# Optimization experiments

Measured on AMD Instinct MI355X. Metric: run time of the kernel, lower is better.

The kernel has to match this reference:

```python
import jax, jax.numpy as jnp
import numpy as np

N = 50000      # nodes
E = 500000     # edges
IN_FEAT = 128
OUT_FEAT = 128
R = 200        # num_relations
NB = 16        # num_bases -> 8x8 blocks
SI = IN_FEAT // NB   # submat_in = 8
SO = OUT_FEAT // NB  # submat_out = 8


def setup_inputs() -> dict:
    key = jax.random.key(0)
    k1, k2, k3, k4, k5, k6, k7 = jax.random.split(key, 7)
    h = jax.random.normal(k1, (N, IN_FEAT), dtype=jnp.float32)
    norm = jax.random.uniform(k2, (N, 1), dtype=jnp.float32)
    weight = jax.random.normal(k3, (R, NB * SI * SO), dtype=jnp.float32) * 0.1
    loop_weight = jax.random.normal(k4, (IN_FEAT, OUT_FEAT), dtype=jnp.float32) * 0.1
    src = jax.random.randint(k5, (E,), 0, N, dtype=jnp.int32)
    dst = jax.random.randint(k6, (E,), 0, N, dtype=jnp.int32)
    etype = jax.random.randint(k7, (E,), 0, R, dtype=jnp.int32)
    return {"h": h, "norm": norm, "weight": weight, "loop_weight": loop_weight,
            "src": src, "dst": dst, "etype": etype}


def reference(h, norm, weight, loop_weight, src, dst, etype):
    # self-loop message: [N, out_feat]
    loop_message = h @ loop_weight
    # per-edge relation-weight gather: [E, NB, SI, SO]
    w_e = weight[etype].reshape(-1, NB, SI, SO)
    # src features as per-basis blocks: [E, NB, SI]
    x_e = h[src].reshape(-1, NB, SI)
    # block-diagonal bmm -> messages [E, out_feat]
    msg = jnp.einsum('ebi,ebio->ebo', x_e, w_e).reshape(-1, OUT_FEAT)
    # scatter-sum to destination nodes (fn.sum(msg -> h))
    agg = jax.ops.segment_sum(msg, dst, num_segments=N)
    # apply_func: multiply by per-node norm, then add self-loop and activation
    nodes = agg * norm
    nodes = nodes + loop_message
    return jax.nn.relu(nodes)
```

## Files before the change

kernel.cpp:

```cpp
#include <hip/hip_runtime.h>
#include <hip/hip_bf16.h>


#define IN_FEAT 128
#define OUT_FEAT 128
#define SCAN_CHUNK 512

using short8  = __attribute__((ext_vector_type(8))) short;
using float4v = __attribute__((ext_vector_type(4))) float;

__device__ inline float blo(unsigned u) { return __uint_as_float(u << 16); }
__device__ inline float bhi(unsigned u) { return __uint_as_float(u & 0xffff0000u); }
__device__ inline unsigned short f2bf(float f) {
  __hip_bfloat16 b = __float2bfloat16(f);
  return *reinterpret_cast<unsigned short*>(&b);
}

__device__ inline float dot2bf(unsigned x, unsigned w, float c) {
#if __has_builtin(__builtin_amdgcn_fdot2_f32_bf16)
  typedef __bf16 bf16x2 __attribute__((ext_vector_type(2)));
  return __builtin_amdgcn_fdot2_f32_bf16(__builtin_bit_cast(bf16x2, x),
                                         __builtin_bit_cast(bf16x2, w), c, false);
#else
  return c + blo(x) * blo(w) + bhi(x) * bhi(w);
#endif
}

__global__ __launch_bounds__(256) void k_prep(
    const float* __restrict__ w, unsigned short* __restrict__ w16, int wtotal,
    const float* __restrict__ h, uint4* __restrict__ h16p, int htotal8,
    const float* __restrict__ lw, unsigned short* __restrict__ lwT,
    const int* __restrict__ dst, int* __restrict__ cnt, int E,
    int bw, int bh, int blw) {
  const int bid = blockIdx.x;
  if (bid < bw) {
    const int idx = bid * 256 + threadIdx.x;
    if (idx < wtotal) {
      const int r = idx >> 10;
      const int rem = idx & 1023;
      const int b = rem >> 6;
      const int q = rem & 63;
      const int opp = q >> 4;
      const int t = q & 15;
      const int j = t >> 3;
      const int i = t & 7;
      w16[idx] = f2bf(w[((size_t)r << 10) + b * 64 + i * 8 + opp * 2 + j]);
    }
  } else if (bid < bw + bh) {
    const int t = (bid - bw) * 256 + threadIdx.x;
    if (t < htotal8) {
      const float4 a = ((const float4*)h)[2 * t];
      const float4 b = ((const float4*)h)[2 * t + 1];
      uint4 o;
      o.x = (unsigned)f2bf(a.x) | ((unsigned)f2bf(a.y) << 16);
      o.y = (unsigned)f2bf(a.z) | ((unsigned)f2bf(a.w) << 16);
      o.z = (unsigned)f2bf(b.x) | ((unsigned)f2bf(b.y) << 16);
      o.w = (unsigned)f2bf(b.z) | ((unsigned)f2bf(b.w) << 16);
      h16p[t] = o;
    }
  } else if (bid < bw + bh + blw) {
    const int idx = (bid - bw - bh) * 256 + threadIdx.x;
    if (idx < IN_FEAT * OUT_FEAT) {
      const int o = idx >> 7;
      const int k = idx & 127;
      lwT[idx] = f2bf(lw[k * 128 + o]);
    }
  } else {
    const int e = (bid - bw - bh - blw) * 256 + threadIdx.x;
    if (e < E) atomicAdd(&cnt[dst[e]], 1);
  }
}

__global__ __launch_bounds__(256) void gemm_mfma(
    const unsigned short* __restrict__ h16, const unsigned short* __restrict__ lwT,
    float* __restrict__ out, int N) {
  const int wid = threadIdx.x >> 6;
  const int lane = threadIdx.x & 63;
  const int row0 = blockIdx.x * 64 + wid * 16;
  if (row0 >= N) return;
  const int m = lane & 15;
  const int kg = (lane >> 4) * 8;
  const int arow = min(row0 + m, N - 1);

  float4v acc[8];
  #pragma unroll
  for (int nt = 0; nt < 8; ++nt) acc[nt] = (float4v){0.f, 0.f, 0.f, 0.f};

  const unsigned short* ap = h16 + (size_t)arow * 128 + kg;
  const unsigned short* bp = lwT + (size_t)m * 128 + kg;

  #pragma unroll
  for (int kc = 0; kc < 4; ++kc) {
    const short8 a = *(const short8*)(ap + kc * 32);
    #pragma unroll
    for (int nt = 0; nt < 8; ++nt) {
      const short8 b = *(const short8*)(bp + nt * 2048 + kc * 32);
      acc[nt] = __builtin_amdgcn_mfma_f32_16x16x32_bf16(a, b, acc[nt], 0, 0, 0);
    }
  }

  const int crow = row0 + (lane >> 4) * 4;
  #pragma unroll
  for (int nt = 0; nt < 8; ++nt) {
    #pragma unroll
    for (int r = 0; r < 4; ++r) {
      const int row = crow + r;
      if (row < N) out[(size_t)row * 128 + nt * 16 + m] = acc[nt][r];
    }
  }
}

__global__ __launch_bounds__(256) void k_hist(
    const int* __restrict__ dst, int* __restrict__ cnt, int E) {
  const int e = blockIdx.x * blockDim.x + threadIdx.x;
  if (e < E) atomicAdd(&cnt[dst[e]], 1);
}

__global__ __launch_bounds__(256) void k_chunksum(
    const int* __restrict__ cnt, int* __restrict__ bsum, int N) {
  __shared__ int s[256];
  const int t = threadIdx.x;
  const int base = blockIdx.x * SCAN_CHUNK;
  int v = 0;
  int i0 = base + t, i1 = base + 256 + t;
  if (i0 < N) v += cnt[i0];
  if (i1 < N) v += cnt[i1];
  s[t] = v;
  __syncthreads();
  for (int d = 128; d > 0; d >>= 1) {
    if (t < d) s[t] += s[t + d];
    __syncthreads();
  }
  if (t == 0) bsum[blockIdx.x] = s[0];
}

__global__ void k_scanb(int* __restrict__ bsum, int nblk) {
  const int lane = threadIdx.x;
  if (nblk <= 128) {
    int o0 = (lane < nblk) ? bsum[lane] : 0;
    int o1 = (64 + lane < nblk) ? bsum[64 + lane] : 0;
    int v0 = o0, v1 = o1;
    #pragma unroll
    for (int d = 1; d < 64; d <<= 1) {
      int t0 = __shfl_up(v0, d);
      int t1 = __shfl_up(v1, d);
      if (lane >= d) { v0 += t0; v1 += t1; }
    }
    const int total0 = __shfl(v0, 63);
    if (lane < nblk) bsum[lane] = v0 - o0;
    if (64 + lane < nblk) bsum[64 + lane] = total0 + v1 - o1;
  } else if (lane == 0) {
    int run = 0;
    for (int b = 0; b < nblk; ++b) { int v = bsum[b]; bsum[b] = run; run += v; }
  }
}

__global__ __launch_bounds__(256) void k_offsets(
    const int* __restrict__ cnt, const int* __restrict__ bsum,
    int* __restrict__ pos, int N) {
  __shared__ int s[256];
  const int t = threadIdx.x;
  const int base = blockIdx.x * SCAN_CHUNK;
  const int i0 = base + 2 * t;
  const int i1 = i0 + 1;
  const int c0 = (i0 < N) ? cnt[i0] : 0;
  const int c1 = (i1 < N) ? cnt[i1] : 0;
  const int pair = c0 + c1;
  s[t] = pair;
  __syncthreads();
  #pragma unroll
  for (int d = 1; d < 256; d <<= 1) {
    int v = (t >= d) ? s[t - d] : 0;
    __syncthreads();
    s[t] += v;
    __syncthreads();
  }
  const int ex = s[t] - pair + bsum[blockIdx.x];
  if (i0 < N) pos[i0] = ex;
  if (i1 < N) pos[i1] = ex + c0;
}

__global__ __launch_bounds__(256) void k_scatter(
    const int* __restrict__ src, const int* __restrict__ dst,
    const int* __restrict__ etype, int* __restrict__ pos,
    int2* __restrict__ srcet, int E) {
  const int e = blockIdx.x * blockDim.x + threadIdx.x;
  if (e < E) {
    const int p = atomicAdd(&pos[dst[e]], 1);
    srcet[p] = make_int2(src[e], etype[e]);
  }
}

__global__ __launch_bounds__(256) void agg_bf16(
    const unsigned short* __restrict__ h16, const float* __restrict__ norm,
    const unsigned short* __restrict__ w16, const int* __restrict__ pos,
    const int* __restrict__ cnt, const int2* __restrict__ srcet,
    float* __restrict__ out, int N) {
  const int node = (int)((blockIdx.x * blockDim.x + threadIdx.x) >> 6);
  const int lane = threadIdx.x & 63;
  if (node >= N) return;

  const int b = lane >> 2;
  const int opp = lane & 3;
  const int woff = b * 64 + opp * 16;
  const int hoff = b * 8;

  const int num = cnt[node];
  const int end = pos[node];
  const int begin = end - num;

  float a0 = 0.f, a1 = 0.f;

  for (int base = 0; base < num; base += 64) {
    const int cn = min(64, num - base);
    const int2 my = srcet[begin + base + min(lane, cn - 1)];
    #pragma unroll 4
    for (int i = 0; i < cn; ++i) {
      const int s = __shfl(my.x, i);
      const int r = __shfl(my.y, i);
      const unsigned short* wp = w16 + ((size_t)r << 10) + woff;
      const uint4 wa = *(const uint4*)(wp);
      const uint4 wb = *(const uint4*)(wp + 8);
      const uint4 xv = *(const uint4*)(h16 + ((size_t)s << 7) + hoff);

      a0 = dot2bf(xv.x, wa.x, a0);
      a0 = dot2bf(xv.y, wa.y, a0);
      a0 = dot2bf(xv.z, wa.z, a0);
      a0 = dot2bf(xv.w, wa.w, a0);
      a1 = dot2bf(xv.x, wb.x, a1);
      a1 = dot2bf(xv.y, wb.y, a1);
      a1 = dot2bf(xv.z, wb.z, a1);
      a1 = dot2bf(xv.w, wb.w, a1);
    }
  }

  const float nm = norm[node];
  const int o = b * 8 + opp * 2;
  float* outp = out + ((size_t)node << 7) + o;
  float2 prev = *(const float2*)outp;
  float2 res;
  res.x = fmaxf(prev.x + a0 * nm, 0.f);
  res.y = fmaxf(prev.y + a1 * nm, 0.f);
  *(float2*)outp = res;
}

__global__ __launch_bounds__(256) void selfloop_gemm(
    const float* __restrict__ h, const float* __restrict__ lw,
    float* __restrict__ out, int n) {
  __shared__ float slw[IN_FEAT * OUT_FEAT];
  __shared__ float sh[32 * IN_FEAT];

  {
    const float4* s4 = (const float4*)lw;
    float4* d4 = (float4*)slw;
    for (int i = threadIdx.x; i < IN_FEAT * OUT_FEAT / 4; i += 256) d4[i] = s4[i];
  }

  const int cg = threadIdx.x & 31;
  const int rg = threadIdx.x >> 5;

  for (int base = blockIdx.x * 32; base < n; base += gridDim.x * 32) {
    const int nrows = min(32, n - base);
    __syncthreads();
    {
      const float4* hs = (const float4*)(h + (size_t)base * IN_FEAT);
      float4* sd = (float4*)sh;
      const int cnt = nrows * (IN_FEAT / 4);
      for (int i = threadIdx.x; i < cnt; i += 256) sd[i] = hs[i];
    }
    __syncthreads();

    float4 acc[4];
    #pragma unroll
    for (int j = 0; j < 4; ++j) acc[j] = make_float4(0.f, 0.f, 0.f, 0.f);

    #pragma unroll 4
    for (int k = 0; k < IN_FEAT; ++k) {
      const float4 w = ((const float4*)slw)[k * 32 + cg];
      #pragma unroll
      for (int j = 0; j < 4; ++j) {
        const float hv = sh[(rg + 8 * j) * IN_FEAT + k];
        acc[j].x += hv * w.x;
        acc[j].y += hv * w.y;
        acc[j].z += hv * w.z;
        acc[j].w += hv * w.w;
      }
    }

    #pragma unroll
    for (int j = 0; j < 4; ++j) {
      const int r = rg + 8 * j;
      if (r < nrows) {
        ((float4*)(out + (size_t)(base + r) * OUT_FEAT))[cg] = acc[j];
      }
    }
  }
}

__global__ __launch_bounds__(256) void agg(
    const float* __restrict__ h, const float* __restrict__ norm,
    const float* __restrict__ weight, const int* __restrict__ pos,
    const int* __restrict__ cnt, const int2* __restrict__ srcet,
    float* __restrict__ out, int N) {
  const int node = (int)((blockIdx.x * blockDim.x + threadIdx.x) >> 6);
  const int lane = threadIdx.x & 63;
  if (node >= N) return;

  const int b = lane >> 2;
  const int op = (lane & 3) * 2;
  const int boff = b * 64 + op;

  const int num = cnt[node];
  const int end = pos[node];
  const int begin = end - num;

  float a0 = 0.f, a1 = 0.f;

  for (int base = 0; base < num; base += 64) {
    const int cn = min(64, num - base);
    const int2 my = srcet[begin + base + min(lane, cn - 1)];
    #pragma unroll 2
    for (int i = 0; i < cn; ++i) {
      const int s = __shfl(my.x, i);
      const int r = __shfl(my.y, i);
      const float* xp = h + ((size_t)s << 7) + b * 8;
      const float4 x0 = ((const float4*)xp)[0];
      const float4 x1 = ((const float4*)xp)[1];
      const float* wp = weight + ((size_t)r << 10) + boff;
      const float2 w0 = *(const float2*)(wp);
      const float2 w1 = *(const float2*)(wp + 8);
      const float2 w2 = *(const float2*)(wp + 16);
      const float2 w3 = *(const float2*)(wp + 24);
      const float2 w4 = *(const float2*)(wp + 32);
      const float2 w5 = *(const float2*)(wp + 40);
      const float2 w6 = *(const float2*)(wp + 48);
      const float2 w7 = *(const float2*)(wp + 56);
      a0 += x0.x * w0.x; a1 += x0.x * w0.y;
      a0 += x0.y * w1.x; a1 += x0.y * w1.y;
      a0 += x0.z * w2.x; a1 += x0.z * w2.y;
      a0 += x0.w * w3.x; a1 += x0.w * w3.y;
      a0 += x1.x * w4.x; a1 += x1.x * w4.y;
      a0 += x1.y * w5.x; a1 += x1.y * w5.y;
      a0 += x1.z * w6.x; a1 += x1.z * w6.y;
      a0 += x1.w * w7.x; a1 += x1.w * w7.y;
    }
  }

  const float nm = norm[node];
  const int o = b * 8 + op;
  float* outp = out + ((size_t)node << 7) + o;
  float2 prev = *(const float2*)outp;
  float2 res;
  res.x = fmaxf(prev.x + a0 * nm, 0.f);
  res.y = fmaxf(prev.y + a1 * nm, 0.f);
  *(float2*)outp = res;
}

__global__ __launch_bounds__(256) void edge_msg(
    const float* __restrict__ h, const float* __restrict__ norm,
    const float* __restrict__ weight, const int* __restrict__ src,
    const int* __restrict__ dst, const int* __restrict__ etype,
    float* out, int E) {
  const int wave = (int)((blockIdx.x * blockDim.x + threadIdx.x) >> 6);
  const int lane = threadIdx.x & 63;
  if (wave >= E) return;

  const int s = src[wave];
  const int d = dst[wave];
  const int r = etype[wave];
  const float nrm = norm[d];

  const int b = lane >> 2;
  const int op = (lane & 3) * 2;

  const float* xp = h + (size_t)s * IN_FEAT + b * 8;
  const float4 x0 = ((const float4*)xp)[0];
  const float4 x1 = ((const float4*)xp)[1];
  float x[8] = {x0.x, x0.y, x0.z, x0.w, x1.x, x1.y, x1.z, x1.w};

  const float* wp = weight + (size_t)r * 1024 + b * 64 + op;
  float a0 = 0.f, a1 = 0.f;
  #pragma unroll
  for (int i = 0; i < 8; ++i) {
    const float2 w = *(const float2*)(wp + i * 8);
    a0 += x[i] * w.x;
    a1 += x[i] * w.y;
  }

  const int o = b * 8 + op;
  float* outp = out + (size_t)d * OUT_FEAT + o;
  atomicAdd(outp, a0 * nrm);
  atomicAdd(outp + 1, a1 * nrm);
}

__global__ __launch_bounds__(256) void relu_k(float* __restrict__ out, int n4) {
  const int i = blockIdx.x * blockDim.x + threadIdx.x;
  if (i < n4) {
    float4 v = ((const float4*)out)[i];
    v.x = fmaxf(v.x, 0.f);
    v.y = fmaxf(v.y, 0.f);
    v.z = fmaxf(v.z, 0.f);
    v.w = fmaxf(v.w, 0.f);
    ((float4*)out)[i] = v;
  }
}

extern "C" void kernel_launch(void* const* d_in, const int* in_sizes, int n_in,
                              void* d_out, int out_size, void* d_ws, size_t ws_size,
                              hipStream_t stream) {
  const float* h    = (const float*)d_in[0];
  const float* norm = (const float*)d_in[1];
  const float* w    = (const float*)d_in[2];
  const float* lw   = (const float*)d_in[3];
  const int* src    = (const int*)d_in[4];
  const int* dst    = (const int*)d_in[5];
  const int* etype  = (const int*)d_in[6];
  float* out = (float*)d_out;

  const int N = in_sizes[1];
  const int E = in_sizes[4];
  const int R = in_sizes[2] / 1024;
  const int nblk = (N + SCAN_CHUNK - 1) / SCAN_CHUNK;

  const size_t nb_bsum = (size_t)((nblk < 128) ? 128 : nblk);
  const size_t off_cnt  = (size_t)E * 8;
  const size_t off_pos  = off_cnt + (size_t)N * 4;
  const size_t off_bsum = off_pos + (size_t)N * 4;
  size_t off_h16 = off_bsum + nb_bsum * 4;
  off_h16 = (off_h16 + 15) & ~(size_t)15;
  const size_t off_w16 = off_h16 + (size_t)N * IN_FEAT * 2;
  const size_t off_lwT = off_w16 + (size_t)R * 1024 * 2;
  const size_t need_full = off_lwT + (size_t)IN_FEAT * OUT_FEAT * 2;
  const size_t need_sort = off_bsum + nb_bsum * 4;

  if (ws_size >= need_full) {
    char* wsb = (char*)d_ws;
    int2* srcet = (int2*)wsb;
    int* cnt  = (int*)(wsb + off_cnt);
    int* pos  = (int*)(wsb + off_pos);
    int* bsum = (int*)(wsb + off_bsum);
    unsigned short* h16 = (unsigned short*)(wsb + off_h16);
    unsigned short* w16 = (unsigned short*)(wsb + off_w16);
    unsigned short* lwT = (unsigned short*)(wsb + off_lwT);

    hipMemsetAsync(cnt, 0, (size_t)N * 4, stream);

    const int wtotal = R * 1024;
    const int htotal8 = N * IN_FEAT / 8;
    const int bw  = (wtotal + 255) / 256;
    const int bh  = (htotal8 + 255) / 256;
    const int blw = (IN_FEAT * OUT_FEAT + 255) / 256;
    const int bhist = (E + 255) / 256;
    k_prep<<<bw + bh + blw + bhist, 256, 0, stream>>>(
        w, w16, wtotal, h, (uint4*)h16, htotal8, lw, lwT, dst, cnt, E,
        bw, bh, blw);

    gemm_mfma<<<(N + 63) / 64, 256, 0, stream>>>(h16, lwT, out, N);

    k_chunksum<<<nblk, 256, 0, stream>>>(cnt, bsum, N);
    k_scanb<<<1, 64, 0, stream>>>(bsum, nblk);
    k_offsets<<<nblk, 256, 0, stream>>>(cnt, bsum, pos, N);
    k_scatter<<<(E + 255) / 256, 256, 0, stream>>>(src, dst, etype, pos, srcet, E);

    agg_bf16<<<(N + 3) / 4, 256, 0, stream>>>(h16, norm, w16, pos, cnt, srcet,
                                              out, N);
  } else if (ws_size >= need_sort) {
    char* wsb = (char*)d_ws;
    int2* srcet = (int2*)wsb;
    int* cnt  = (int*)(wsb + off_cnt);
    int* pos  = (int*)(wsb + off_pos);
    int* bsum = (int*)(wsb + off_bsum);

    selfloop_gemm<<<512, 256, 0, stream>>>(h, lw, out, N);
    hipMemsetAsync(cnt, 0, (size_t)N * 4, stream);
    k_hist<<<(E + 255) / 256, 256, 0, stream>>>(dst, cnt, E);
    k_chunksum<<<nblk, 256, 0, stream>>>(cnt, bsum, N);
    k_scanb<<<1, 64, 0, stream>>>(bsum, nblk);
    k_offsets<<<nblk, 256, 0, stream>>>(cnt, bsum, pos, N);
    k_scatter<<<(E + 255) / 256, 256, 0, stream>>>(src, dst, etype, pos, srcet, E);
    agg<<<(N + 3) / 4, 256, 0, stream>>>(h, norm, w, pos, cnt, srcet, out, N);
  } else {
    selfloop_gemm<<<512, 256, 0, stream>>>(h, lw, out, N);
    edge_msg<<<(E + 3) / 4, 256, 0, stream>>>(h, norm, w, src, dst, etype, out, E);
    const int n4 = N * OUT_FEAT / 4;
    relu_k<<<(n4 + 255) / 256, 256, 0, stream>>>(out, n4);
  }
}
```

Before: 152.1 us.

## Split per-node aggregation across four waves, each handling four bases and four edges

The bf16 aggregation kernel now assigns one 256-thread block per destination node instead of one wave per node. Each wave covers four of the sixteen bases, and within a wave four 16-lane groups each take a different edge. Partial sums are combined with xor shuffles before one group writes the result. This shortens the serial edge loop per node (about 10 edges on average) to expose more memory parallelism. In exchange it launches four times as many waves, adds masked padding iterations and reduction shuffles, and leaves more lanes idle at the tail.

```diff
diff --git a/kernel.cpp b/kernel.cpp
--- a/kernel.cpp
+++ b/kernel.cpp
@@ -191,17 +191,19 @@
   }
 }
 
-__global__ __launch_bounds__(256) void agg_bf16(
+__global__ __launch_bounds__(256) void agg_bf16_q(
     const unsigned short* __restrict__ h16, const float* __restrict__ norm,
     const unsigned short* __restrict__ w16, const int* __restrict__ pos,
     const int* __restrict__ cnt, const int2* __restrict__ srcet,
     float* __restrict__ out, int N) {
-  const int node = (int)((blockIdx.x * blockDim.x + threadIdx.x) >> 6);
+  const int node = blockIdx.x;
+  if (node >= N) return;
+  const int quarter = threadIdx.x >> 6;
   const int lane = threadIdx.x & 63;
-  if (node >= N) return;
-
-  const int b = lane >> 2;
+  const int sub = lane >> 4;
+  const int b4  = (lane >> 2) & 3;
   const int opp = lane & 3;
+  const int b = quarter * 4 + b4;
   const int woff = b * 64 + opp * 16;
   const int hoff = b * 8;
 
@@ -214,14 +216,18 @@
   for (int base = 0; base < num; base += 64) {
     const int cn = min(64, num - base);
     const int2 my = srcet[begin + base + min(lane, cn - 1)];
-    #pragma unroll 4
-    for (int i = 0; i < cn; ++i) {
-      const int s = __shfl(my.x, i);
-      const int r = __shfl(my.y, i);
+    const int iters = (cn + 3) >> 2;
+    #pragma unroll 2
+    for (int it = 0; it < iters; ++it) {
+      const int ei = it * 4 + sub;
+      const int srcl = min(ei, cn - 1);
+      const int s = __shfl(my.x, srcl);
+      const int r = __shfl(my.y, srcl);
       const unsigned short* wp = w16 + ((size_t)r << 10) + woff;
       const uint4 wa = *(const uint4*)(wp);
       const uint4 wb = *(const uint4*)(wp + 8);
-      const uint4 xv = *(const uint4*)(h16 + ((size_t)s << 7) + hoff);
+      uint4 xv = *(const uint4*)(h16 + ((size_t)s << 7) + hoff);
+      if (ei >= cn) { xv.x = 0u; xv.y = 0u; xv.z = 0u; xv.w = 0u; }
 
       a0 = dot2bf(xv.x, wa.x, a0);
       a0 = dot2bf(xv.y, wa.y, a0);
@@ -234,14 +240,21 @@
     }
   }
 
-  const float nm = norm[node];
-  const int o = b * 8 + opp * 2;
-  float* outp = out + ((size_t)node << 7) + o;
-  float2 prev = *(const float2*)outp;
-  float2 res;
-  res.x = fmaxf(prev.x + a0 * nm, 0.f);
-  res.y = fmaxf(prev.y + a1 * nm, 0.f);
-  *(float2*)outp = res;
+  a0 += __shfl_xor(a0, 16);
+  a0 += __shfl_xor(a0, 32);
+  a1 += __shfl_xor(a1, 16);
+  a1 += __shfl_xor(a1, 32);
+
+  if (lane < 16) {
+    const float nm = norm[node];
+    const int o = b * 8 + opp * 2;
+    float* outp = out + ((size_t)node << 7) + o;
+    const float2 prev = *(const float2*)outp;
+    float2 res;
+    res.x = fmaxf(prev.x + a0 * nm, 0.f);
+    res.y = fmaxf(prev.y + a1 * nm, 0.f);
+    *(float2*)outp = res;
+  }
 }
 
 __global__ __launch_bounds__(256) void selfloop_gemm(
@@ -462,8 +475,7 @@
     k_offsets<<<nblk, 256, 0, stream>>>(cnt, bsum, pos, N);
     k_scatter<<<(E + 255) / 256, 256, 0, stream>>>(src, dst, etype, pos, srcet, E);
 
-    agg_bf16<<<(N + 3) / 4, 256, 0, stream>>>(h16, norm, w16, pos, cnt, srcet,
-                                              out, N);
+    agg_bf16_q<<<N, 256, 0, stream>>>(h16, norm, w16, pos, cnt, srcet, out, N);
   } else if (ws_size >= need_sort) {
     char* wsb = (char*)d_ws;
     int2* srcet = (int2*)wsb;
```

Result: slower. 175.1 us (+15.1%).

## Fuse GEMM with chunk sums, drop scan kernel, split node edges across two waves

Applied to the files above, without the earlier changes.

The self-loop MFMA GEMM and the per-chunk count reduction now run in one launch, using separate block ranges. The single-block scan kernel is removed: each offsets block sums the preceding chunk totals itself with a 64-lane reduction. The aggregation kernel now gives each node two waves that take alternating edges, then combines the partial sums through shared memory. This cuts launch overhead and raises edge-level parallelism, at the cost of a block sync and redundant prefix reads.

```diff
diff --git a/kernel.cpp b/kernel.cpp
--- a/kernel.cpp
+++ b/kernel.cpp
@@ -71,49 +71,62 @@
   }
 }
 
-__global__ __launch_bounds__(256) void gemm_mfma(
+__global__ __launch_bounds__(256) void k_gemm_sum(
     const unsigned short* __restrict__ h16, const unsigned short* __restrict__ lwT,
-    float* __restrict__ out, int N) {
-  const int wid = threadIdx.x >> 6;
-  const int lane = threadIdx.x & 63;
-  const int row0 = blockIdx.x * 64 + wid * 16;
-  if (row0 >= N) return;
-  const int m = lane & 15;
-  const int kg = (lane >> 4) * 8;
-  const int arow = min(row0 + m, N - 1);
-
-  float4v acc[8];
-  #pragma unroll
-  for (int nt = 0; nt < 8; ++nt) acc[nt] = (float4v){0.f, 0.f, 0.f, 0.f};
-
-  const unsigned short* ap = h16 + (size_t)arow * 128 + kg;
-  const unsigned short* bp = lwT + (size_t)m * 128 + kg;
-
-  #pragma unroll
-  for (int kc = 0; kc < 4; ++kc) {
-    const short8 a = *(const short8*)(ap + kc * 32);
+    float* __restrict__ out, int N,
+    const int* __restrict__ cnt, int* __restrict__ bsum, int gemm_blocks) {
+  if (blockIdx.x < gemm_blocks) {
+    const int wid = threadIdx.x >> 6;
+    const int lane = threadIdx.x & 63;
+    const int row0 = blockIdx.x * 64 + wid * 16;
+    if (row0 >= N) return;
+    const int m = lane & 15;
+    const int kg = (lane >> 4) * 8;
+    const int arow = min(row0 + m, N - 1);
+
+    float4v acc[8];
+    #pragma unroll
+    for (int nt = 0; nt < 8; ++nt) acc[nt] = (float4v){0.f, 0.f, 0.f, 0.f};
+
+    const unsigned short* ap = h16 + (size_t)arow * 128 + kg;
+    const unsigned short* bp = lwT + (size_t)m * 128 + kg;
+
+    #pragma unroll
+    for (int kc = 0; kc < 4; ++kc) {
+      const short8 a = *(const short8*)(ap + kc * 32);
+      #pragma unroll
+      for (int nt = 0; nt < 8; ++nt) {
+        const short8 b = *(const short8*)(bp + nt * 2048 + kc * 32);
+        acc[nt] = __builtin_amdgcn_mfma_f32_16x16x32_bf16(a, b, acc[nt], 0, 0, 0);
+      }
+    }
+
+    const int crow = row0 + (lane >> 4) * 4;
     #pragma unroll
     for (int nt = 0; nt < 8; ++nt) {
-      const short8 b = *(const short8*)(bp + nt * 2048 + kc * 32);
-      acc[nt] = __builtin_amdgcn_mfma_f32_16x16x32_bf16(a, b, acc[nt], 0, 0, 0);
-    }
-  }
-
-  const int crow = row0 + (lane >> 4) * 4;
-  #pragma unroll
-  for (int nt = 0; nt < 8; ++nt) {
-    #pragma unroll
-    for (int r = 0; r < 4; ++r) {
-      const int row = crow + r;
-      if (row < N) out[(size_t)row * 128 + nt * 16 + m] = acc[nt][r];
-    }
-  }
-}
-
-__global__ __launch_bounds__(256) void k_hist(
-    const int* __restrict__ dst, int* __restrict__ cnt, int E) {
-  const int e = blockIdx.x * blockDim.x + threadIdx.x;
-  if (e < E) atomicAdd(&cnt[dst[e]], 1);
+      #pragma unroll
+      for (int r = 0; r < 4; ++r) {
+        const int row = crow + r;
+        if (row < N) out[(size_t)row * 128 + nt * 16 + m] = acc[nt][r];
+      }
+    }
+  } else {
+    __shared__ int s[256];
+    const int cb = blockIdx.x - gemm_blocks;
+    const int t = threadIdx.x;
+    const int base = cb * SCAN_CHUNK;
+    int v = 0;
+    const int i0 = base + t, i1 = base + 256 + t;
+    if (i0 < N) v += cnt[i0];
+    if (i1 < N) v += cnt[i1];
+    s[t] = v;
+    __syncthreads();
+    for (int d = 128; d > 0; d >>= 1) {
+      if (t < d) s[t] += s[t + d];
+      __syncthreads();
+    }
+    if (t == 0) bsum[cb] = s[0];
+  }
 }
 
 __global__ __launch_bounds__(256) void k_chunksum(
@@ -134,32 +147,25 @@
   if (t == 0) bsum[blockIdx.x] = s[0];
 }
 
-__global__ void k_scanb(int* __restrict__ bsum, int nblk) {
-  const int lane = threadIdx.x;
-  if (nblk <= 128) {
-    int o0 = (lane < nblk) ? bsum[lane] : 0;
-    int o1 = (64 + lane < nblk) ? bsum[64 + lane] : 0;
-    int v0 = o0, v1 = o1;
-    #pragma unroll
-    for (int d = 1; d < 64; d <<= 1) {
-      int t0 = __shfl_up(v0, d);
-      int t1 = __shfl_up(v1, d);
-      if (lane >= d) { v0 += t0; v1 += t1; }
-    }
-    const int total0 = __shfl(v0, 63);
-    if (lane < nblk) bsum[lane] = v0 - o0;
-    if (64 + lane < nblk) bsum[64 + lane] = total0 + v1 - o1;
-  } else if (lane == 0) {
-    int run = 0;
-    for (int b = 0; b < nblk; ++b) { int v = bsum[b]; bsum[b] = run; run += v; }
-  }
+__global__ __launch_bounds__(256) void k_hist(
+    const int* __restrict__ dst, int* __restrict__ cnt, int E) {
+  const int e = blockIdx.x * blockDim.x + threadIdx.x;
+  if (e < E) atomicAdd(&cnt[dst[e]], 1);
 }
 
 __global__ __launch_bounds__(256) void k_offsets(
     const int* __restrict__ cnt, const int* __restrict__ bsum,
     int* __restrict__ pos, int N) {
   __shared__ int s[256];
+  __shared__ int sbase;
   const int t = threadIdx.x;
+  if (t < 64) {
+    int acc = 0;
+    for (int j = t; j < (int)blockIdx.x; j += 64) acc += bsum[j];
+    #pragma unroll
+    for (int d = 1; d < 64; d <<= 1) acc += __shfl_xor(acc, d);
+    if (t == 0) sbase = acc;
+  }
   const int base = blockIdx.x * SCAN_CHUNK;
   const int i0 = base + 2 * t;
   const int i1 = i0 + 1;
@@ -175,7 +181,7 @@
     s[t] += v;
     __syncthreads();
   }
-  const int ex = s[t] - pair + bsum[blockIdx.x];
+  const int ex = s[t] - pair + sbase;
   if (i0 < N) pos[i0] = ex;
   if (i1 < N) pos[i1] = ex + c0;
 }
@@ -191,57 +197,67 @@
   }
 }
 
-__global__ __launch_bounds__(256) void agg_bf16(
+__global__ __launch_bounds__(256) void agg_bf16_2w(
     const unsigned short* __restrict__ h16, const float* __restrict__ norm,
     const unsigned short* __restrict__ w16, const int* __restrict__ pos,
     const int* __restrict__ cnt, const int2* __restrict__ srcet,
     float* __restrict__ out, int N) {
-  const int node = (int)((blockIdx.x * blockDim.x + threadIdx.x) >> 6);
+  __shared__ float red[2][128];
+  const int wid = threadIdx.x >> 6;
   const int lane = threadIdx.x & 63;
-  if (node >= N) return;
+  const int sub = wid >> 1;
+  const int half = wid & 1;
+  const int node = blockIdx.x * 2 + sub;
 
   const int b = lane >> 2;
   const int opp = lane & 3;
   const int woff = b * 64 + opp * 16;
   const int hoff = b * 8;
-
-  const int num = cnt[node];
-  const int end = pos[node];
-  const int begin = end - num;
+  const int o = b * 8 + opp * 2;
 
   float a0 = 0.f, a1 = 0.f;
-
-  for (int base = 0; base < num; base += 64) {
-    const int cn = min(64, num - base);
-    const int2 my = srcet[begin + base + min(lane, cn - 1)];
-    #pragma unroll 4
-    for (int i = 0; i < cn; ++i) {
-      const int s = __shfl(my.x, i);
-      const int r = __shfl(my.y, i);
-      const unsigned short* wp = w16 + ((size_t)r << 10) + woff;
-      const uint4 wa = *(const uint4*)(wp);
-      const uint4 wb = *(const uint4*)(wp + 8);
-      const uint4 xv = *(const uint4*)(h16 + ((size_t)s << 7) + hoff);
-
-      a0 = dot2bf(xv.x, wa.x, a0);
-      a0 = dot2bf(xv.y, wa.y, a0);
-      a0 = dot2bf(xv.z, wa.z, a0);
-      a0 = dot2bf(xv.w, wa.w, a0);
-      a1 = dot2bf(xv.x, wb.x, a1);
-      a1 = dot2bf(xv.y, wb.y, a1);
-      a1 = dot2bf(xv.z, wb.z, a1);
-      a1 = dot2bf(xv.w, wb.w, a1);
-    }
-  }
-
-  const float nm = norm[node];
-  const int o = b * 8 + opp * 2;
-  float* outp = out + ((size_t)node << 7) + o;
-  float2 prev = *(const float2*)outp;
-  float2 res;
-  res.x = fmaxf(prev.x + a0 * nm, 0.f);
-  res.y = fmaxf(prev.y + a1 * nm, 0.f);
-  *(float2*)outp = res;
+  if (node < N) {
+    const int num = cnt[node];
+    const int end = pos[node];
+    const int begin = end - num;
+    for (int base = 0; base < num; base += 64) {
+      const int cn = min(64, num - base);
+      const int2 my = srcet[begin + base + min(lane, cn - 1)];
+      #pragma unroll 2
+      for (int i = half; i < cn; i += 2) {
+        const int s = __shfl(my.x, i);
+        const int r = __shfl(my.y, i);
+        const unsigned short* wp = w16 + ((size_t)r << 10) + woff;
+        const uint4 wa = *(const uint4*)(wp);
+        const uint4 wb = *(const uint4*)(wp + 8);
+        const uint4 xv = *(const uint4*)(h16 + ((size_t)s << 7) + hoff);
+
+        a0 = dot2bf(xv.x, wa.x, a0);
+        a0 = dot2bf(xv.y, wa.y, a0);
+        a0 = dot2bf(xv.z, wa.z, a0);
+        a0 = dot2bf(xv.w, wa.w, a0);
+        a1 = dot2bf(xv.x, wb.x, a1);
+        a1 = dot2bf(xv.y, wb.y, a1);
+        a1 = dot2bf(xv.z, wb.z, a1);
+        a1 = dot2bf(xv.w, wb.w, a1);
+      }
+    }
+  }
+
+  if (half == 1) {
+    *(float2*)&red[sub][o] = make_float2(a0, a1);
+  }
+  __syncthreads();
+  if (half == 0 && node < N) {
+    const float2 other = *(const float2*)&red[sub][o];
+    const float nm = norm[node];
+    float* outp = out + ((size_t)node << 7) + o;
+    const float2 prev = *(const float2*)outp;
+    float2 res;
+    res.x = fmaxf(prev.x + (a0 + other.x) * nm, 0.f);
+    res.y = fmaxf(prev.y + (a1 + other.y) * nm, 0.f);
+    *(float2*)outp = res;
+  }
 }
 
 __global__ __launch_bounds__(256) void selfloop_gemm(
@@ -455,15 +471,15 @@
         w, w16, wtotal, h, (uint4*)h16, htotal8, lw, lwT, dst, cnt, E,
         bw, bh, blw);
 
-    gemm_mfma<<<(N + 63) / 64, 256, 0, stream>>>(h16, lwT, out, N);
-
-    k_chunksum<<<nblk, 256, 0, stream>>>(cnt, bsum, N);
-    k_scanb<<<1, 64, 0, stream>>>(bsum, nblk);
+    const int gemm_blocks = (N + 63) / 64;
+    k_gemm_sum<<<gemm_blocks + nblk, 256, 0, stream>>>(
+        h16, lwT, out, N, cnt, bsum, gemm_blocks);
+
     k_offsets<<<nblk, 256, 0, stream>>>(cnt, bsum, pos, N);
     k_scatter<<<(E + 255) / 256, 256, 0, stream>>>(src, dst, etype, pos, srcet, E);
 
-    agg_bf16<<<(N + 3) / 4, 256, 0, stream>>>(h16, norm, w16, pos, cnt, srcet,
-                                              out, N);
+    agg_bf16_2w<<<(N + 1) / 2, 256, 0, stream>>>(h16, norm, w16, pos, cnt,
+                                                 srcet, out, N);
   } else if (ws_size >= need_sort) {
     char* wsb = (char*)d_ws;
     int2* srcet = (int2*)wsb;
@@ -475,7 +491,6 @@
     hipMemsetAsync(cnt, 0, (size_t)N * 4, stream);
     k_hist<<<(E + 255) / 256, 256, 0, stream>>>(dst, cnt, E);
     k_chunksum<<<nblk, 256, 0, stream>>>(cnt, bsum, N);
-    k_scanb<<<1, 64, 0, stream>>>(bsum, nblk);
     k_offsets<<<nblk, 256, 0, stream>>>(cnt, bsum, pos, N);
     k_scatter<<<(E + 255) / 256, 256, 0, stream>>>(src, dst, etype, pos, srcet, E);
     agg<<<(N + 3) / 4, 256, 0, stream>>>(h, norm, w, pos, cnt, srcet, out, N);
```

New measurement: 152.2 us. Within noise of the previous version (+0.0%).
